# Kernel optimization log

Hardware: AMD Instinct MI355X
Metric: run time of the kernel (lower is better)

Reference implementation:

```python
import jax, jax.numpy as jnp
import numpy as np

B, S, H = 4, 2048, 1024
E = 8
INTER = 2816  # round(4.0*1024*2/3)=2731 -> next multiple of 256


def setup_inputs() -> dict:
    key = jax.random.key(0)
    k1, k2, k3, k4 = jax.random.split(key, 4)
    x = jax.random.normal(k1, (B, S, H), dtype=jnp.float32)
    gate_w = jax.random.normal(k2, (E, H), dtype=jnp.float32) * 0.02
    w_gate_up = jax.random.normal(k3, (E, H, 2 * INTER), dtype=jnp.float32) * 0.02
    w_down = jax.random.normal(k4, (E, INTER, H), dtype=jnp.float32) * 0.02
    return {"x": x, "gate_w": gate_w, "w_gate_up": w_gate_up, "w_down": w_down, "top_k": 2}


def _moe(x, gate_w, w_gate_up, w_down, top_k):
    Bx, Sx, Hx = x.shape
    Ex = gate_w.shape[0]
    T = Bx * Sx
    # Router
    logits = jnp.einsum('bsh,eh->bse', x, gate_w)
    probs = jax.nn.softmax(logits.astype(jnp.float32), axis=-1)  # [B,S,E] fp32
    topk_vals, topk_idx = jax.lax.top_k(probs, top_k)             # [B,S,K]
    topk_w = topk_vals / jnp.clip(topk_vals.sum(-1, keepdims=True), 1e-8)
    importance = probs.mean((0, 1))                               # [E]
    onehot = jax.nn.one_hot(topk_idx, Ex, dtype=probs.dtype)      # [B,S,K,E]
    sel_mask = onehot.sum(-2)                                     # [B,S,E] 0/1 (topk unique)
    load = sel_mask.sum((0, 1)) / (T * top_k)
    aux_loss = (Ex * (importance * load)).sum()
    # Dense combine weights per token/expert (scatter_add equivalent)
    W_full = (onehot * topk_w[..., None]).sum(-2)                 # [B,S,E]
    x_flat = x.reshape(T, Hx)
    W_flat = W_full.reshape(T, Ex).astype(x.dtype)
    out = jnp.zeros_like(x_flat)
    for e in range(Ex):  # fixed small expert loop
        gu = x_flat @ w_gate_up[e]                                # [T, 2I]
        g, u = jnp.split(gu, 2, axis=-1)
        y = (jax.nn.silu(g) * u) @ w_down[e]                      # [T, H]
        out = out + y * W_flat[:, e:e + 1]
    return out.reshape(Bx, Sx, Hx), aux_loss


def reference(x, gate_w, w_gate_up, w_down, top_k):
    return _moe(x, gate_w, w_gate_up, w_down, int(top_k))
```

## Files before the change

### kernel.cpp

```cpp
#include <hip/hip_runtime.h>

#define E_ 8
#define H_ 1024
#define I_ 2816
#define GU_ 5632
#define T_ 8192
#define NBR_ 2048

typedef __attribute__((ext_vector_type(8))) __bf16 bf16x8;
typedef __attribute__((ext_vector_type(4))) float f32x4;
typedef __attribute__((ext_vector_type(8))) unsigned short u16x8;
typedef unsigned short u16;

__device__ __forceinline__ float bf2f(u16 u) {
  union { unsigned int i; float f; } v; v.i = ((unsigned int)u) << 16; return v.f;
}
__device__ __forceinline__ u16 f2bf(float f) {
  union { float f; unsigned int i; } v; v.f = f;
  unsigned int r = v.i + 0x7fffu + ((v.i >> 16) & 1u);
  return (u16)(r >> 16);
}
__device__ __forceinline__ void gld16(const void* g, void* l) {
  __builtin_amdgcn_global_load_lds((const __attribute__((address_space(1))) void*)g,
                                   (__attribute__((address_space(3))) void*)l, 16, 0, 0);
}

__global__ __launch_bounds__(256) void k_router(
    const float* __restrict__ x, const float* __restrict__ gw,
    float* __restrict__ part_imp, int* __restrict__ part_cnt,
    int* __restrict__ tok_e, float* __restrict__ tok_w,
    u16* __restrict__ xb)
{
  __shared__ float s_imp[8];
  __shared__ int s_cnt[8];
  if (threadIdx.x < 8) { s_imp[threadIdx.x] = 0.f; s_cnt[threadIdx.x] = 0; }
  __syncthreads();

  const int t = blockIdx.x * 4 + (threadIdx.x >> 6);
  const int lane = threadIdx.x & 63;
  const float* xr = x + (size_t)t * H_;
  const f32x4* xp = (const f32x4*)(xr + lane * 16);
  f32x4 v0 = xp[0], v1 = xp[1], v2 = xp[2], v3 = xp[3];
  float xv[16];
#pragma unroll
  for (int b = 0; b < 4; ++b) { xv[b] = v0[b]; xv[4+b] = v1[b]; xv[8+b] = v2[b]; xv[12+b] = v3[b]; }
  u16x8 o0, o1;
#pragma unroll
  for (int j = 0; j < 8; ++j) { o0[j] = f2bf(xv[j]); o1[j] = f2bf(xv[8 + j]); }
  *(u16x8*)(xb + (size_t)t * H_ + lane * 16) = o0;
  *(u16x8*)(xb + (size_t)t * H_ + lane * 16 + 8) = o1;

  float lg[8];
#pragma unroll
  for (int e = 0; e < 8; ++e) {
    const f32x4* gp = (const f32x4*)(gw + e * H_ + lane * 16);
    float s = 0.f;
#pragma unroll
    for (int a = 0; a < 4; ++a) {
      f32x4 g4 = gp[a];
#pragma unroll
      for (int b = 0; b < 4; ++b) s += xv[a * 4 + b] * g4[b];
    }
    lg[e] = s;
  }
#pragma unroll
  for (int e = 0; e < 8; ++e)
#pragma unroll
    for (int off = 32; off; off >>= 1) lg[e] += __shfl_xor(lg[e], off);

  float m = lg[0];
#pragma unroll
  for (int e = 1; e < 8; ++e) m = fmaxf(m, lg[e]);
  float p[8], sum = 0.f;
#pragma unroll
  for (int e = 0; e < 8; ++e) { p[e] = __expf(lg[e] - m); sum += p[e]; }
  float inv = 1.f / sum;
#pragma unroll
  for (int e = 0; e < 8; ++e) p[e] *= inv;
  int e0 = 0;
#pragma unroll
  for (int e = 1; e < 8; ++e) if (p[e] > p[e0]) e0 = e;
  int e1 = (e0 == 0) ? 1 : 0;
#pragma unroll
  for (int e = 0; e < 8; ++e) if (e != e0 && p[e] > p[e1]) e1 = e;
  float d = 1.f / (p[e0] + p[e1]);
  if (lane == 0) {
#pragma unroll
    for (int e = 0; e < 8; ++e) atomicAdd(&s_imp[e], p[e]);
    atomicAdd(&s_cnt[e0], 1);
    atomicAdd(&s_cnt[e1], 1);
    tok_e[2 * t] = e0; tok_e[2 * t + 1] = e1;
    tok_w[2 * t] = p[e0] * d; tok_w[2 * t + 1] = p[e1] * d;
  }
  __syncthreads();
  if (threadIdx.x < 8) {
    part_imp[blockIdx.x * 8 + threadIdx.x] = s_imp[threadIdx.x];
    part_cnt[blockIdx.x * 8 + threadIdx.x] = s_cnt[threadIdx.x];
  }
}

__global__ __launch_bounds__(512) void k_reduce_scan(
    const float* __restrict__ part_imp, const int* __restrict__ part_cnt,
    int* __restrict__ counts, int* __restrict__ offsets, float* __restrict__ out)
{
  const int w = threadIdx.x >> 6, lane = threadIdx.x & 63;
  float si = 0.f; int sc = 0;
  for (int b = lane; b < NBR_; b += 64) { si += part_imp[b * 8 + w]; sc += part_cnt[b * 8 + w]; }
#pragma unroll
  for (int off = 32; off; off >>= 1) { si += __shfl_xor(si, off); sc += __shfl_xor(sc, off); }
  __shared__ float fimp[8];
  __shared__ int fcnt[8];
  if (lane == 0) { fimp[w] = si; fcnt[w] = sc; }
  __syncthreads();
  if (threadIdx.x == 0) {
    int off = 0; float aux = 0.f;
#pragma unroll
    for (int e = 0; e < 8; ++e) {
      counts[e] = fcnt[e]; offsets[e] = off; off += fcnt[e];
      aux += fimp[e] * (float)fcnt[e];
    }
    out[(size_t)T_ * H_] = 8.f * aux / ((float)T_ * (float)(2 * T_));
  }
}

__global__ __launch_bounds__(256) void k_scatter(
    const int* __restrict__ tok_e, const float* __restrict__ tok_w,
    const int* __restrict__ offsets, int* __restrict__ cursors,
    int* __restrict__ rows, float* __restrict__ wslot, int* __restrict__ t2s)
{
  __shared__ int lcnt[8], lbase[8];
  if (threadIdx.x < 8) lcnt[threadIdx.x] = 0;
  __syncthreads();
  const int t = blockIdx.x * 256 + threadIdx.x;
  const int e0 = tok_e[2 * t], e1 = tok_e[2 * t + 1];
  const int p0 = atomicAdd(&lcnt[e0], 1);
  const int p1 = atomicAdd(&lcnt[e1], 1);
  __syncthreads();
  if (threadIdx.x < 8) lbase[threadIdx.x] = atomicAdd(&cursors[threadIdx.x], lcnt[threadIdx.x]);
  __syncthreads();
  const int s0 = offsets[e0] + lbase[e0] + p0;
  const int s1 = offsets[e1] + lbase[e1] + p1;
  rows[s0] = t; wslot[s0] = tok_w[2 * t];     t2s[2 * t] = s0;
  rows[s1] = t; wslot[s1] = tok_w[2 * t + 1]; t2s[2 * t + 1] = s1;
}

__global__ __launch_bounds__(256) void k_transpose(
    const float* __restrict__ src, u16* __restrict__ dst, int R, int C)
{
  __shared__ float tile[32][33];
  const int z = blockIdx.z;
  const int c0 = blockIdx.x * 32, r0 = blockIdx.y * 32;
  const float* s = src + (size_t)z * R * C;
  u16* d = dst + (size_t)z * R * C;
  const int tx = threadIdx.x & 31, ty = threadIdx.x >> 5;
#pragma unroll
  for (int i = 0; i < 4; ++i)
    tile[ty + i * 8][tx] = s[(size_t)(r0 + ty + i * 8) * C + c0 + tx];
  __syncthreads();
#pragma unroll
  for (int i = 0; i < 4; ++i)
    d[(size_t)(c0 + ty + i * 8) * R + r0 + tx] = f2bf(tile[tx][ty + i * 8]);
}

__global__ __launch_bounds__(512, 2) void k_gemm1(
    const u16* __restrict__ xb, const u16* __restrict__ wgu_t,
    const int* __restrict__ counts, const int* __restrict__ offsets,
    const int* __restrict__ rows, const float* __restrict__ wslot,
    u16* __restrict__ act)
{
  extern __shared__ char sh[];
  const int bid = blockIdx.x;
  const int l = (bid & 7) * 704 + (bid >> 3);
  const int e = l / 704;
  const int rm = l - e * 704;
  const int y = rm >> 5, x = rm & 31;
  const int cnt = counts[e];
  const int m0 = x * 256;
  if (m0 >= cnt) return;
  const int seg = offsets[e];
  const int segLast = seg + cnt - 1;
  const int n0 = y * 128;

  const int tid = threadIdx.x;
  const int wid = tid >> 6, lane = tid & 63;
  const int srow = tid >> 3;
  const int scol = (tid & 7) * 8;

  const u16* wge = wgu_t + (size_t)e * GU_ * H_;

  int tA[4];
#pragma unroll
  for (int i = 0; i < 4; ++i) {
    int slot = seg + m0 + i * 64 + srow;
    tA[i] = rows[slot > segLast ? segLast : slot];
  }
  const u16* bSrc[4];
#pragma unroll
  for (int i = 0; i < 4; ++i) {
    int r = i * 64 + srow;
    int gr = (r < 128) ? (n0 + r) : (I_ + n0 + (r - 128));
    bSrc[i] = wge + (size_t)gr * H_;
  }

  const int wm = (wid >> 2) * 128;
  const int wn = (wid & 3) * 32;

  f32x4 accg[8][2], accu[8][2];
#pragma unroll
  for (int i = 0; i < 8; ++i)
#pragma unroll
    for (int j = 0; j < 2; ++j) { accg[i][j] = (f32x4){0.f,0.f,0.f,0.f}; accu[i][j] = (f32x4){0.f,0.f,0.f,0.f}; }

#define STAGE1(b, kt)                                                             \
  {                                                                               \
    const int k0 = (kt) * 64;                                                     \
    char* base = sh + (b) * 65536 + wid * 1024;                                   \
    _Pragma("unroll")                                                             \
    for (int i = 0; i < 4; ++i)                                                   \
      gld16(xb + (size_t)tA[i] * H_ + k0 + scol, base + i * 8192);                \
    _Pragma("unroll")                                                             \
    for (int i = 0; i < 4; ++i)                                                   \
      gld16(bSrc[i] + k0 + scol, base + 32768 + i * 8192);                        \
  }

  STAGE1(0, 0);
  __syncthreads();
  int cur = 0;
  for (int kt = 0; kt < 16; ++kt) {
    if (kt < 15) STAGE1(cur ^ 1, kt + 1);
    const u16* At = (const u16*)(sh + cur * 65536);
    const u16* Bt = At + 16384;
#pragma unroll
    for (int ks = 0; ks < 2; ++ks) {
      const int kk = ks * 32 + (lane >> 4) * 8;
      bf16x8 a[8], bg[2], bu[2];
#pragma unroll
      for (int mf = 0; mf < 8; ++mf)
        a[mf] = *(const bf16x8*)(At + (wm + mf * 16 + (lane & 15)) * 64 + kk);
#pragma unroll
      for (int nf = 0; nf < 2; ++nf) {
        bg[nf] = *(const bf16x8*)(Bt + (wn + nf * 16 + (lane & 15)) * 64 + kk);
        bu[nf] = *(const bf16x8*)(Bt + (128 + wn + nf * 16 + (lane & 15)) * 64 + kk);
      }
#pragma unroll
      for (int mf = 0; mf < 8; ++mf)
#pragma unroll
        for (int nf = 0; nf < 2; ++nf) {
          accg[mf][nf] = __builtin_amdgcn_mfma_f32_16x16x32_bf16(a[mf], bg[nf], accg[mf][nf], 0, 0, 0);
          accu[mf][nf] = __builtin_amdgcn_mfma_f32_16x16x32_bf16(a[mf], bu[nf], accu[mf][nf], 0, 0, 0);
        }
    }
    __syncthreads();
    cur ^= 1;
  }

#pragma unroll
  for (int mf = 0; mf < 8; ++mf)
#pragma unroll
    for (int reg = 0; reg < 4; ++reg) {
      const int r = wm + mf * 16 + (lane >> 4) * 4 + reg;
      if (m0 + r >= cnt) continue;
      const int slot = seg + m0 + r;
      const float w = wslot[slot];
#pragma unroll
      for (int nf = 0; nf < 2; ++nf) {
        float g = accg[mf][nf][reg];
        float u = accu[mf][nf][reg];
        float sv = (g / (1.f + __expf(-g))) * u * w;
        act[(size_t)slot * I_ + n0 + wn + nf * 16 + (lane & 15)] = f2bf(sv);
      }
    }
#undef STAGE1
}

__global__ __launch_bounds__(512, 2) void k_gemm2(
    const u16* __restrict__ act, const u16* __restrict__ wd_t,
    const int* __restrict__ counts, const int* __restrict__ offsets,
    u16* __restrict__ y)
{
  extern __shared__ char sh[];
  const int bid = blockIdx.x;
  const int l = (bid & 7) * 256 + (bid >> 3);
  const int e = l >> 8;
  const int yb = (l >> 5) & 7, x = l & 31;
  const int cnt = counts[e];
  const int m0 = x * 256;
  if (m0 >= cnt) return;
  const int seg = offsets[e];
  const int segLast = seg + cnt - 1;
  const int n0 = yb * 128;

  const int tid = threadIdx.x;
  const int wid = tid >> 6, lane = tid & 63;
  const int srow = tid >> 3, scol = (tid & 7) * 8;

  const u16* wde = wd_t + (size_t)e * H_ * I_;

  int aS[4];
#pragma unroll
  for (int i = 0; i < 4; ++i) {
    int slot = seg + m0 + i * 64 + srow;
    aS[i] = slot > segLast ? segLast : slot;
  }
  const u16* bSrc[2];
#pragma unroll
  for (int i = 0; i < 2; ++i)
    bSrc[i] = wde + (size_t)(n0 + i * 64 + srow) * I_;

  const int wm = (wid >> 2) * 128;
  const int wn = (wid & 3) * 32;

  f32x4 acc[8][2];
#pragma unroll
  for (int i = 0; i < 8; ++i)
#pragma unroll
    for (int j = 0; j < 2; ++j) acc[i][j] = (f32x4){0.f,0.f,0.f,0.f};

#define STAGE2(b, kt)                                                             \
  {                                                                               \
    const int k0 = (kt) * 64;                                                     \
    char* base = sh + (b) * 49152 + wid * 1024;                                   \
    _Pragma("unroll")                                                             \
    for (int i = 0; i < 4; ++i)                                                   \
      gld16(act + (size_t)aS[i] * I_ + k0 + scol, base + i * 8192);               \
    _Pragma("unroll")                                                             \
    for (int i = 0; i < 2; ++i)                                                   \
      gld16(bSrc[i] + k0 + scol, base + 32768 + i * 8192);                        \
  }

  STAGE2(0, 0);
  __syncthreads();
  int cur = 0;
  for (int kt = 0; kt < 44; ++kt) {
    if (kt < 43) STAGE2(cur ^ 1, kt + 1);
    const u16* At = (const u16*)(sh + cur * 49152);
    const u16* Bt = At + 16384;
#pragma unroll
    for (int ks = 0; ks < 2; ++ks) {
      const int kk = ks * 32 + (lane >> 4) * 8;
      bf16x8 a[8], b[2];
#pragma unroll
      for (int mf = 0; mf < 8; ++mf)
        a[mf] = *(const bf16x8*)(At + (wm + mf * 16 + (lane & 15)) * 64 + kk);
#pragma unroll
      for (int nf = 0; nf < 2; ++nf)
        b[nf] = *(const bf16x8*)(Bt + (wn + nf * 16 + (lane & 15)) * 64 + kk);
#pragma unroll
      for (int mf = 0; mf < 8; ++mf)
#pragma unroll
        for (int nf = 0; nf < 2; ++nf)
          acc[mf][nf] = __builtin_amdgcn_mfma_f32_16x16x32_bf16(a[mf], b[nf], acc[mf][nf], 0, 0, 0);
    }
    __syncthreads();
    cur ^= 1;
  }

#pragma unroll
  for (int mf = 0; mf < 8; ++mf)
#pragma unroll
    for (int reg = 0; reg < 4; ++reg) {
      const int r = wm + mf * 16 + (lane >> 4) * 4 + reg;
      if (m0 + r >= cnt) continue;
      const int slot = seg + m0 + r;
#pragma unroll
      for (int nf = 0; nf < 2; ++nf)
        y[(size_t)slot * H_ + n0 + wn + nf * 16 + (lane & 15)] = f2bf(acc[mf][nf][reg]);
    }
#undef STAGE2
}

__global__ __launch_bounds__(256) void k_combine(
    const u16* __restrict__ y, const int* __restrict__ t2s, float* __restrict__ out)
{
  const size_t idx = ((size_t)blockIdx.x * 256 + threadIdx.x) * 8;
  const int t = (int)(idx >> 10);
  const int h = (int)(idx & 1023);
  const int s0 = t2s[2 * t], s1 = t2s[2 * t + 1];
  u16x8 a = *(const u16x8*)(y + (size_t)s0 * H_ + h);
  u16x8 b = *(const u16x8*)(y + (size_t)s1 * H_ + h);
  f32x4 o0, o1;
#pragma unroll
  for (int j = 0; j < 4; ++j) o0[j] = bf2f(a[j]) + bf2f(b[j]);
#pragma unroll
  for (int j = 0; j < 4; ++j) o1[j] = bf2f(a[4 + j]) + bf2f(b[4 + j]);
  *(f32x4*)(out + idx) = o0;
  *(f32x4*)(out + idx + 4) = o1;
}

extern "C" void kernel_launch(void* const* d_in, const int* in_sizes, int n_in,
                              void* d_out, int out_size, void* d_ws, size_t ws_size,
                              hipStream_t stream)
{
  const float* x   = (const float*)d_in[0];
  const float* gw  = (const float*)d_in[1];
  const float* wgu = (const float*)d_in[2];
  const float* wd  = (const float*)d_in[3];
  float* out = (float*)d_out;
  char* ws = (char*)d_ws;

  const size_t off_wgu_t = 0;
  const size_t off_wd_t  = off_wgu_t + (size_t)E_ * GU_ * H_ * 2;
  const size_t off_xb    = off_wd_t  + (size_t)E_ * H_ * I_ * 2;
  const size_t off_act   = off_xb    + (size_t)T_ * H_ * 2;
  const size_t off_ctrl  = off_act   + (size_t)2 * T_ * I_ * 2;
  const size_t need = off_ctrl + 128 + 5 * 65536;
  if (ws_size < need) return;

  u16* wgu_t = (u16*)(ws + off_wgu_t);
  u16* wd_t  = (u16*)(ws + off_wd_t);
  u16* xb    = (u16*)(ws + off_xb);
  u16* act   = (u16*)(ws + off_act);
  u16* y     = (u16*)(ws + off_wgu_t);
  float* part_imp = (float*)(ws + off_act);
  int*   part_cnt = (int*)(ws + off_act + (size_t)NBR_ * 8 * 4);
  char* ctrl = ws + off_ctrl;
  int*   counts  = (int*)(ctrl + 0);
  int*   cursors = (int*)(ctrl + 32);
  int*   offsets = (int*)(ctrl + 64);
  int*   tok_e   = (int*)(ctrl + 128);
  float* tok_w   = (float*)(ctrl + 128 + 1 * 65536);
  int*   rows    = (int*)(ctrl + 128 + 2 * 65536);
  float* wslot   = (float*)(ctrl + 128 + 3 * 65536);
  int*   t2s     = (int*)(ctrl + 128 + 4 * 65536);

  static bool attr_done = false;
  if (!attr_done) {
    hipFuncSetAttribute((const void*)k_gemm1, hipFuncAttributeMaxDynamicSharedMemorySize, 131072);
    hipFuncSetAttribute((const void*)k_gemm2, hipFuncAttributeMaxDynamicSharedMemorySize, 98304);
    attr_done = true;
  }

  hipMemsetAsync(ctrl, 0, 96, stream);
  hipLaunchKernelGGL(k_transpose, dim3(GU_ / 32, H_ / 32, E_), dim3(256), 0, stream, wgu, wgu_t, H_, GU_);
  hipLaunchKernelGGL(k_transpose, dim3(H_ / 32, I_ / 32, E_), dim3(256), 0, stream, wd, wd_t, I_, H_);
  hipLaunchKernelGGL(k_router, dim3(NBR_), dim3(256), 0, stream, x, gw, part_imp, part_cnt, tok_e, tok_w, xb);
  hipLaunchKernelGGL(k_reduce_scan, dim3(1), dim3(512), 0, stream, part_imp, part_cnt, counts, offsets, out);
  hipLaunchKernelGGL(k_scatter, dim3(T_ / 256), dim3(256), 0, stream, tok_e, tok_w, offsets, cursors, rows, wslot, t2s);
  hipLaunchKernelGGL(k_gemm1, dim3(32 * (I_ / 128) * E_), dim3(512), 131072, stream, xb, wgu_t, counts, offsets, rows, wslot, act);
  hipLaunchKernelGGL(k_gemm2, dim3(32 * (H_ / 128) * E_), dim3(512), 98304, stream, act, wd_t, counts, offsets, y);
  hipLaunchKernelGGL(k_combine, dim3((T_ * H_) / (256 * 8)), dim3(256), 0, stream, y, t2s, out);
}
```

Baseline: 655.7 us.

## Swizzle LDS tiles, split A/B prefetch stages, widen gemm2 N tile

Both grouped GEMMs now XOR-swizzle the LDS column layout on global_load_lds writes and fragment reads, which is meant to remove bank conflicts. The loop is restructured so the B tile prefetches one step ahead and the A tile two steps ahead, with explicit vmcnt waits and raw barriers replacing __syncthreads. MFMA sections are wrapped in s_setprio to favor the math waves. gemm2 doubles its N tile to 256, which halves the block count and raises register use per wave, and the reworked synchronisation risks subtle races.

Result: faster. 546.5 us (-16.6%).

```diff
diff --git a/kernel.cpp b/kernel.cpp
--- a/kernel.cpp
+++ b/kernel.cpp
@@ -173,33 +173,33 @@
   const int l = (bid & 7) * 704 + (bid >> 3);
   const int e = l / 704;
   const int rm = l - e * 704;
-  const int y = rm >> 5, x = rm & 31;
+  const int yb = rm >> 5, xx = rm & 31;
   const int cnt = counts[e];
-  const int m0 = x * 256;
+  const int m0 = xx * 256;
   if (m0 >= cnt) return;
   const int seg = offsets[e];
   const int segLast = seg + cnt - 1;
-  const int n0 = y * 128;
+  const int n0 = yb * 128;
 
   const int tid = threadIdx.x;
   const int wid = tid >> 6, lane = tid & 63;
   const int srow = tid >> 3;
-  const int scol = (tid & 7) * 8;
+  const int scol = (((tid & 7) ^ (srow & 7)) * 8);
 
   const u16* wge = wgu_t + (size_t)e * GU_ * H_;
 
-  int tA[4];
+  const u16* aPtr[4];
 #pragma unroll
   for (int i = 0; i < 4; ++i) {
     int slot = seg + m0 + i * 64 + srow;
-    tA[i] = rows[slot > segLast ? segLast : slot];
-  }
-  const u16* bSrc[4];
+    aPtr[i] = xb + (size_t)rows[slot > segLast ? segLast : slot] * H_ + scol;
+  }
+  const u16* bPtr[4];
 #pragma unroll
   for (int i = 0; i < 4; ++i) {
     int r = i * 64 + srow;
     int gr = (r < 128) ? (n0 + r) : (I_ + n0 + (r - 128));
-    bSrc[i] = wge + (size_t)gr * H_;
+    bPtr[i] = wge + (size_t)gr * H_ + scol;
   }
 
   const int wm = (wid >> 2) * 128;
@@ -211,37 +211,37 @@
 #pragma unroll
     for (int j = 0; j < 2; ++j) { accg[i][j] = (f32x4){0.f,0.f,0.f,0.f}; accu[i][j] = (f32x4){0.f,0.f,0.f,0.f}; }
 
-#define STAGE1(b, kt)                                                             \
-  {                                                                               \
-    const int k0 = (kt) * 64;                                                     \
-    char* base = sh + (b) * 65536 + wid * 1024;                                   \
-    _Pragma("unroll")                                                             \
-    for (int i = 0; i < 4; ++i)                                                   \
-      gld16(xb + (size_t)tA[i] * H_ + k0 + scol, base + i * 8192);                \
-    _Pragma("unroll")                                                             \
-    for (int i = 0; i < 4; ++i)                                                   \
-      gld16(bSrc[i] + k0 + scol, base + 32768 + i * 8192);                        \
-  }
-
-  STAGE1(0, 0);
-  __syncthreads();
+#define STAGE_A1(b, kt) { const int k0 = (kt) * 64;                               \
+    char* dst = sh + (b) * 65536 + tid * 16;                                      \
+    _Pragma("unroll") for (int i = 0; i < 4; ++i) gld16(aPtr[i] + k0, dst + i * 8192); }
+#define STAGE_B1(b, kt) { const int k0 = (kt) * 64;                               \
+    char* dst = sh + (b) * 65536 + 32768 + tid * 16;                              \
+    _Pragma("unroll") for (int i = 0; i < 4; ++i) gld16(bPtr[i] + k0, dst + i * 8192); }
+
+  const int NT = H_ / 64;
+  STAGE_A1(0, 0); STAGE_B1(0, 0); STAGE_A1(1, 1);
+  asm volatile("s_waitcnt vmcnt(4)" ::: "memory");
+  __builtin_amdgcn_s_barrier();
+
   int cur = 0;
-  for (int kt = 0; kt < 16; ++kt) {
-    if (kt < 15) STAGE1(cur ^ 1, kt + 1);
-    const u16* At = (const u16*)(sh + cur * 65536);
-    const u16* Bt = At + 16384;
+#pragma unroll 2
+  for (int t = 0; t < NT; ++t) {
+    STAGE_B1(cur ^ 1, (t + 1 < NT) ? t + 1 : NT - 1);
+    const u16* As = (const u16*)(sh + cur * 65536);
+    const u16* Bs = As + 16384;
 #pragma unroll
     for (int ks = 0; ks < 2; ++ks) {
-      const int kk = ks * 32 + (lane >> 4) * 8;
+      const int koff = (ks * 32 + (lane >> 4) * 8) ^ ((lane & 7) * 8);
       bf16x8 a[8], bg[2], bu[2];
 #pragma unroll
       for (int mf = 0; mf < 8; ++mf)
-        a[mf] = *(const bf16x8*)(At + (wm + mf * 16 + (lane & 15)) * 64 + kk);
+        a[mf] = *(const bf16x8*)(As + (wm + mf * 16 + (lane & 15)) * 64 + koff);
 #pragma unroll
       for (int nf = 0; nf < 2; ++nf) {
-        bg[nf] = *(const bf16x8*)(Bt + (wn + nf * 16 + (lane & 15)) * 64 + kk);
-        bu[nf] = *(const bf16x8*)(Bt + (128 + wn + nf * 16 + (lane & 15)) * 64 + kk);
+        bg[nf] = *(const bf16x8*)(Bs + (wn + nf * 16 + (lane & 15)) * 64 + koff);
+        bu[nf] = *(const bf16x8*)(Bs + (128 + wn + nf * 16 + (lane & 15)) * 64 + koff);
       }
+      __builtin_amdgcn_s_setprio(1);
 #pragma unroll
       for (int mf = 0; mf < 8; ++mf)
 #pragma unroll
@@ -249,10 +249,18 @@
           accg[mf][nf] = __builtin_amdgcn_mfma_f32_16x16x32_bf16(a[mf], bg[nf], accg[mf][nf], 0, 0, 0);
           accu[mf][nf] = __builtin_amdgcn_mfma_f32_16x16x32_bf16(a[mf], bu[nf], accu[mf][nf], 0, 0, 0);
         }
-    }
-    __syncthreads();
+      __builtin_amdgcn_s_setprio(0);
+    }
+    asm volatile("" ::: "memory");
+    __builtin_amdgcn_s_barrier();
+    STAGE_A1(cur, (t + 2 < NT) ? t + 2 : NT - 1);
+    asm volatile("s_waitcnt vmcnt(4)" ::: "memory");
+    __builtin_amdgcn_s_barrier();
     cur ^= 1;
   }
+  asm volatile("s_waitcnt vmcnt(0)" ::: "memory");
+#undef STAGE_A1
+#undef STAGE_B1
 
 #pragma unroll
   for (int mf = 0; mf < 8; ++mf)
@@ -270,7 +278,6 @@
         act[(size_t)slot * I_ + n0 + wn + nf * 16 + (lane & 15)] = f2bf(sv);
       }
     }
-#undef STAGE1
 }
 
 __global__ __launch_bounds__(512, 2) void k_gemm2(
@@ -280,80 +287,90 @@
 {
   extern __shared__ char sh[];
   const int bid = blockIdx.x;
-  const int l = (bid & 7) * 256 + (bid >> 3);
-  const int e = l >> 8;
-  const int yb = (l >> 5) & 7, x = l & 31;
+  const int l = (bid & 7) * 128 + (bid >> 3);
+  const int e = l >> 7;
+  const int rm = l & 127;
+  const int yb = rm >> 5, xx = rm & 31;
   const int cnt = counts[e];
-  const int m0 = x * 256;
+  const int m0 = xx * 256;
   if (m0 >= cnt) return;
   const int seg = offsets[e];
   const int segLast = seg + cnt - 1;
-  const int n0 = yb * 128;
+  const int n0 = yb * 256;
 
   const int tid = threadIdx.x;
   const int wid = tid >> 6, lane = tid & 63;
-  const int srow = tid >> 3, scol = (tid & 7) * 8;
+  const int srow = tid >> 3;
+  const int scol = (((tid & 7) ^ (srow & 7)) * 8);
 
   const u16* wde = wd_t + (size_t)e * H_ * I_;
 
-  int aS[4];
+  const u16* aPtr[4];
 #pragma unroll
   for (int i = 0; i < 4; ++i) {
     int slot = seg + m0 + i * 64 + srow;
-    aS[i] = slot > segLast ? segLast : slot;
-  }
-  const u16* bSrc[2];
-#pragma unroll
-  for (int i = 0; i < 2; ++i)
-    bSrc[i] = wde + (size_t)(n0 + i * 64 + srow) * I_;
+    aPtr[i] = act + (size_t)(slot > segLast ? segLast : slot) * I_ + scol;
+  }
+  const u16* bPtr[4];
+#pragma unroll
+  for (int i = 0; i < 4; ++i)
+    bPtr[i] = wde + (size_t)(n0 + i * 64 + srow) * I_ + scol;
 
   const int wm = (wid >> 2) * 128;
-  const int wn = (wid & 3) * 32;
-
-  f32x4 acc[8][2];
+  const int wn = (wid & 3) * 64;
+
+  f32x4 acc[8][4];
 #pragma unroll
   for (int i = 0; i < 8; ++i)
 #pragma unroll
-    for (int j = 0; j < 2; ++j) acc[i][j] = (f32x4){0.f,0.f,0.f,0.f};
-
-#define STAGE2(b, kt)                                                             \
-  {                                                                               \
-    const int k0 = (kt) * 64;                                                     \
-    char* base = sh + (b) * 49152 + wid * 1024;                                   \
-    _Pragma("unroll")                                                             \
-    for (int i = 0; i < 4; ++i)                                                   \
-      gld16(act + (size_t)aS[i] * I_ + k0 + scol, base + i * 8192);               \
-    _Pragma("unroll")                                                             \
-    for (int i = 0; i < 2; ++i)                                                   \
-      gld16(bSrc[i] + k0 + scol, base + 32768 + i * 8192);                        \
-  }
-
-  STAGE2(0, 0);
-  __syncthreads();
+    for (int j = 0; j < 4; ++j) acc[i][j] = (f32x4){0.f,0.f,0.f,0.f};
+
+#define STAGE_A2(b, kt) { const int k0 = (kt) * 64;                               \
+    char* dst = sh + (b) * 65536 + tid * 16;                                      \
+    _Pragma("unroll") for (int i = 0; i < 4; ++i) gld16(aPtr[i] + k0, dst + i * 8192); }
+#define STAGE_B2(b, kt) { const int k0 = (kt) * 64;                               \
+    char* dst = sh + (b) * 65536 + 32768 + tid * 16;                              \
+    _Pragma("unroll") for (int i = 0; i < 4; ++i) gld16(bPtr[i] + k0, dst + i * 8192); }
+
+  const int NT = I_ / 64;
+  STAGE_A2(0, 0); STAGE_B2(0, 0); STAGE_A2(1, 1);
+  asm volatile("s_waitcnt vmcnt(4)" ::: "memory");
+  __builtin_amdgcn_s_barrier();
+
   int cur = 0;
-  for (int kt = 0; kt < 44; ++kt) {
-    if (kt < 43) STAGE2(cur ^ 1, kt + 1);
-    const u16* At = (const u16*)(sh + cur * 49152);
-    const u16* Bt = At + 16384;
+#pragma unroll 2
+  for (int t = 0; t < NT; ++t) {
+    STAGE_B2(cur ^ 1, (t + 1 < NT) ? t + 1 : NT - 1);
+    const u16* As = (const u16*)(sh + cur * 65536);
+    const u16* Bs = As + 16384;
 #pragma unroll
     for (int ks = 0; ks < 2; ++ks) {
-      const int kk = ks * 32 + (lane >> 4) * 8;
-      bf16x8 a[8], b[2];
+      const int koff = (ks * 32 + (lane >> 4) * 8) ^ ((lane & 7) * 8);
+      bf16x8 a[8], b[4];
 #pragma unroll
       for (int mf = 0; mf < 8; ++mf)
-        a[mf] = *(const bf16x8*)(At + (wm + mf * 16 + (lane & 15)) * 64 + kk);
-#pragma unroll
-      for (int nf = 0; nf < 2; ++nf)
-        b[nf] = *(const bf16x8*)(Bt + (wn + nf * 16 + (lane & 15)) * 64 + kk);
+        a[mf] = *(const bf16x8*)(As + (wm + mf * 16 + (lane & 15)) * 64 + koff);
+#pragma unroll
+      for (int nf = 0; nf < 4; ++nf)
+        b[nf] = *(const bf16x8*)(Bs + (wn + nf * 16 + (lane & 15)) * 64 + koff);
+      __builtin_amdgcn_s_setprio(1);
 #pragma unroll
       for (int mf = 0; mf < 8; ++mf)
 #pragma unroll
-        for (int nf = 0; nf < 2; ++nf)
+        for (int nf = 0; nf < 4; ++nf)
           acc[mf][nf] = __builtin_amdgcn_mfma_f32_16x16x32_bf16(a[mf], b[nf], acc[mf][nf], 0, 0, 0);
-    }
-    __syncthreads();
+      __builtin_amdgcn_s_setprio(0);
+    }
+    asm volatile("" ::: "memory");
+    __builtin_amdgcn_s_barrier();
+    STAGE_A2(cur, (t + 2 < NT) ? t + 2 : NT - 1);
+    asm volatile("s_waitcnt vmcnt(4)" ::: "memory");
+    __builtin_amdgcn_s_barrier();
     cur ^= 1;
   }
+  asm volatile("s_waitcnt vmcnt(0)" ::: "memory");
+#undef STAGE_A2
+#undef STAGE_B2
 
 #pragma unroll
   for (int mf = 0; mf < 8; ++mf)
@@ -363,10 +380,9 @@
       if (m0 + r >= cnt) continue;
       const int slot = seg + m0 + r;
 #pragma unroll
-      for (int nf = 0; nf < 2; ++nf)
+      for (int nf = 0; nf < 4; ++nf)
         y[(size_t)slot * H_ + n0 + wn + nf * 16 + (lane & 15)] = f2bf(acc[mf][nf][reg]);
     }
-#undef STAGE2
 }
 
 __global__ __launch_bounds__(256) void k_combine(
@@ -426,7 +442,7 @@
   static bool attr_done = false;
   if (!attr_done) {
     hipFuncSetAttribute((const void*)k_gemm1, hipFuncAttributeMaxDynamicSharedMemorySize, 131072);
-    hipFuncSetAttribute((const void*)k_gemm2, hipFuncAttributeMaxDynamicSharedMemorySize, 98304);
+    hipFuncSetAttribute((const void*)k_gemm2, hipFuncAttributeMaxDynamicSharedMemorySize, 131072);
     attr_done = true;
   }
 
@@ -437,6 +453,6 @@
   hipLaunchKernelGGL(k_reduce_scan, dim3(1), dim3(512), 0, stream, part_imp, part_cnt, counts, offsets, out);
   hipLaunchKernelGGL(k_scatter, dim3(T_ / 256), dim3(256), 0, stream, tok_e, tok_w, offsets, cursors, rows, wslot, t2s);
   hipLaunchKernelGGL(k_gemm1, dim3(32 * (I_ / 128) * E_), dim3(512), 131072, stream, xb, wgu_t, counts, offsets, rows, wslot, act);
-  hipLaunchKernelGGL(k_gemm2, dim3(32 * (H_ / 128) * E_), dim3(512), 98304, stream, act, wd_t, counts, offsets, y);
+  hipLaunchKernelGGL(k_gemm2, dim3(32 * (H_ / 256) * E_), dim3(512), 131072, stream, act, wd_t, counts, offsets, y);
   hipLaunchKernelGGL(k_combine, dim3((T_ * H_) / (256 * 8)), dim3(256), 0, stream, y, t2s, out);
 }
```
